# Kernel tuning notes

Hardware: AMD Instinct MI355X
Metric: run time of the kernel (lower is better)

## Reference

```python
import jax, jax.numpy as jnp
import numpy as np

B, S, H, M, STEPS = 8, 1024, 1024, 4, 5
LN_EPS = 1e-5


def _gelu(x):
    return jax.nn.gelu(x, approximate=False)  # torch nn.GELU default is exact erf


def _layernorm(x, g, b):
    mu = jnp.mean(x, axis=-1, keepdims=True)
    var = jnp.mean((x - mu) ** 2, axis=-1, keepdims=True)
    return (x - mu) * jax.lax.rsqrt(var + LN_EPS) * g + b


def setup_inputs() -> dict:
    key = jax.random.key(0)
    ks = jax.random.split(key, 16)
    def w(k, shape, scale=0.02):
        return (jax.random.normal(k, shape) * scale).astype(jnp.float32)
    z = lambda *shape: jnp.zeros(shape, jnp.float32)
    o = lambda *shape: jnp.ones(shape, jnp.float32)
    return {
        "deterministic_state": jax.random.normal(ks[0], (B, S, H), jnp.float32),
        "superposition_state": jax.random.normal(ks[1], (B, S, H * M), jnp.float32),
        "context": jax.random.normal(ks[2], (B, H), jnp.float32),
        # reasoning_mode_selector: Linear(H,H) -> GELU -> Linear(H,2) -> Softmax
        "Wm1": w(ks[3], (H, H)), "bm1": z(H), "Wm2": w(ks[4], (H, 2)), "bm2": z(2),
        # reasoning_depth_controller: Linear(H,H//2) -> GELU -> Linear(H//2,STEPS) -> Softmax
        "Wd1": w(ks[5], (H, H // 2)), "bd1": z(H // 2), "Wd2": w(ks[6], (H // 2, STEPS)), "bd2": z(STEPS),
        # explicit_reasoning_steps (stacked over STEPS): Linear(2H,H)->GELU->Linear(H,H)->LayerNorm
        "We1": w(ks[7], (STEPS, 2 * H, H)), "be1": z(STEPS, H),
        "We2": w(ks[8], (STEPS, H, H)), "be2": z(STEPS, H),
        "ln_g": o(STEPS, H), "ln_b": z(STEPS, H),
        # reasoning_memory GRUCell(H,H); gate order r,z,n as in torch
        "W_ih": w(ks[9], (H, 3 * H)), "W_hh": w(ks[10], (H, 3 * H)),
        "b_ih": z(3 * H), "b_hh": z(3 * H),
        # implicit_reasoning: Linear(H*M,2H)->GELU->Linear(2H,H*M)->LayerNorm
        "Wi1": w(ks[11], (H * M, 2 * H)), "bi1": z(2 * H),
        "Wi2": w(ks[12], (2 * H, H * M)), "bi2": z(H * M),
        "lni_g": o(H * M), "lni_b": z(H * M),
    }


def _forward(deterministic_state, superposition_state, context,
             Wm1, bm1, Wm2, bm2, Wd1, bd1, Wd2, bd2,
             We1, be1, We2, be2, ln_g, ln_b,
             W_ih, W_hh, b_ih, b_hh,
             Wi1, bi1, Wi2, bi2, lni_g, lni_b):
    b, s, h = deterministic_state.shape
    # mode / depth selection from 2D context [B,H]
    mode_weights = jax.nn.softmax(_gelu(context @ Wm1 + bm1) @ Wm2 + bm2, axis=-1)   # [B,2]
    depth_weights = jax.nn.softmax(_gelu(context @ Wd1 + bd1) @ Wd2 + bd2, axis=-1)  # [B,STEPS]

    ctx_exp = jnp.broadcast_to(context[:, None, :], (b, s, h))  # context.unsqueeze(1).expand

    def gru_cell(x, hprev):  # x,hprev: [N,H]
        gi = x @ W_ih + b_ih
        gh = hprev @ W_hh + b_hh
        i_r, i_z, i_n = jnp.split(gi, 3, axis=-1)
        h_r, h_z, h_n = jnp.split(gh, 3, axis=-1)
        r = jax.nn.sigmoid(i_r + h_r)
        z = jax.nn.sigmoid(i_z + h_z)
        n = jnp.tanh(i_n + r * h_n)
        return (1.0 - z) * n + z * hprev

    def step(carry, params):
        state, memory = carry
        W1, b1, W2, b2, g, beta = params
        combined = jnp.concatenate([state, ctx_exp], axis=-1)          # [B,S,2H]
        next_state = _layernorm(_gelu(combined @ W1 + b1) @ W2 + b2, g, beta)
        mem = gru_cell(next_state.reshape(-1, h), memory.reshape(-1, h)).reshape(b, s, h)
        gated = next_state + 0.1 * mem
        return (gated, mem), gated

    init = (deterministic_state, jnp.zeros_like(deterministic_state))
    _, gated_states = jax.lax.scan(step, init, (We1, be1, We2, be2, ln_g, ln_b))  # [STEPS,B,S,H]
    explicit_result = jnp.einsum('bi,ibsh->bsh', depth_weights, gated_states)

    implicit_result = _layernorm(_gelu(superposition_state @ Wi1 + bi1) @ Wi2 + bi2, lni_g, lni_b)  # [B,S,M*H]
    implicit_det = implicit_result.reshape(b, s, M, h).mean(axis=2)  # [B,S,H]

    result = (mode_weights[:, 0, None, None] * implicit_det
              + mode_weights[:, 1, None, None] * explicit_result)
    return result, mode_weights, depth_weights, explicit_result, implicit_result


def reference(deterministic_state, superposition_state, context,
              Wm1, bm1, Wm2, bm2, Wd1, bd1, Wd2, bd2,
              We1, be1, We2, be2, ln_g, ln_b,
              W_ih, W_hh, b_ih, b_hh,
              Wi1, bi1, Wi2, bi2, lni_g, lni_b):
    return _forward(deterministic_state, superposition_state, context,
                    Wm1, bm1, Wm2, bm2, Wd1, bd1, Wd2, bd2,
                    We1, be1, We2, be2, ln_g, ln_b,
                    W_ih, W_hh, b_ih, b_hh,
                    Wi1, bi1, Wi2, bi2, lni_g, lni_b)
```

## Files before the change

### kernel.cpp

```cpp
#include <hip/hip_runtime.h>
#include <hip/hip_bf16.h>
#include <math.h>


typedef unsigned short bf16_t;
typedef __attribute__((ext_vector_type(8))) short s8v;
typedef __attribute__((ext_vector_type(4))) float f4v;

typedef const __attribute__((address_space(1))) void* gas_ptr;
typedef __attribute__((address_space(3))) void* las_ptr;

#define DEVFN static __device__ __forceinline__

DEVFN bf16_t f2b(float f) {
    union { float f; unsigned u; } v; v.f = f;
    unsigned r = v.u + 0x7FFFu + ((v.u >> 16) & 1u);
    return (bf16_t)(r >> 16);
}
DEVFN float b2f(bf16_t b) {
    union { unsigned u; float f; } v; v.u = ((unsigned)b) << 16; return v.f;
}
DEVFN float geluf(float x) { return 0.5f * x * (1.0f + erff(x * 0.70710678118654752f)); }
DEVFN float sigmf(float x) { return 1.0f / (1.0f + expf(-x)); }

static const long OUT_RESULT = 0;
static const long OUT_MODE   = 8388608;
static const long OUT_DEPTH  = 8388624;
static const long OUT_EXPL   = 8388664;
static const long OUT_IMPL   = 16777272;

#define READ_A(h, c_) { _Pragma("unroll") \
    for (int mf = 0; mf < MF / 2; ++mf) { _Pragma("unroll") \
      for (int ks = 0; ks < 2; ++ks) { \
        aA[h][mf][ks] = *(const s8v*)(lds + (c_) * BUFB + \
            (arow_base + ((h) * (MF / 2) + mf) * 16) * 128 + \
            ((((ks << 2) + lhi) ^ l7) << 4)); } } }

#define READ_B(h, c_) { _Pragma("unroll") \
    for (int nf = 0; nf < NF / 2; ++nf) { _Pragma("unroll") \
      for (int ks = 0; ks < 2; ++ks) { \
        bB[h][nf][ks] = *(const s8v*)(lds + (c_) * BUFB + ABYTES + \
            (brow_base + ((h) * (NF / 2) + nf) * 16) * 128 + \
            ((((ks << 2) + lhi) ^ l7) << 4)); } } }

#define MFMAQ(mh, nh) { __builtin_amdgcn_s_setprio(1); _Pragma("unroll") \
    for (int mf = 0; mf < MF / 2; ++mf) { _Pragma("unroll") \
      for (int nf = 0; nf < NF / 2; ++nf) { _Pragma("unroll") \
        for (int ks = 0; ks < 2; ++ks) { \
          acc[(mh) * (MF / 2) + mf][(nh) * (NF / 2) + nf] = \
            __builtin_amdgcn_mfma_f32_16x16x32_bf16(aA[mh][mf][ks], bB[nh][nf][ks], \
                acc[(mh) * (MF / 2) + mf][(nh) * (NF / 2) + nf], 0, 0, 0); } } } \
    __builtin_amdgcn_s_setprio(0); }

#define WAIT_VM_LPT() { if (LPT == 8) asm volatile("s_waitcnt vmcnt(8)" ::: "memory"); \
                        else          asm volatile("s_waitcnt vmcnt(6)" ::: "memory"); }

template <int MF, int NF, int EPI>
__global__ __launch_bounds__(512, 2) void gemm8p(
    const bf16_t* __restrict__ A, const bf16_t* __restrict__ Bt,
    const float* __restrict__ bias, bf16_t* __restrict__ outB, int N, int K)
{
    constexpr int BM = MF * 32;
    constexpr int BN = NF * 64;
    constexpr int LA = BM / 64;
    constexpr int LB = BN / 64;
    constexpr int LPT = LA + LB;
    constexpr int ABYTES = BM * 128;
    constexpr int BUFB = (BM + BN) * 128;

    __shared__ __align__(16) char lds[2 * BUFB];

    const int tid  = threadIdx.x;
    const int lane = tid & 63;
    const int wave = tid >> 6;
    const int wm = wave >> 2, wn = wave & 3;
    const int l15 = lane & 15, lhi = lane >> 4, l7 = lane & 7;

    const int gx = gridDim.x;
    const int nwg = gx * gridDim.y;
    const int orig = blockIdx.y * gx + blockIdx.x;
    const int qq = nwg >> 3, rr8 = nwg & 7;
    const int xcd = orig & 7, lid = orig >> 3;
    const int nid = (xcd < rr8 ? xcd * (qq + 1) : rr8 * (qq + 1) + (xcd - rr8) * qq) + lid;
    const int m0 = (nid / gx) * BM;
    const int n0 = (nid % gx) * BN;

    const int NT = K >> 6;

    const int arow_base = wm * (BM / 2) + l15;
    const int brow_base = wn * (NF * 16) + l15;

    f4v acc[MF][NF];
#pragma unroll
    for (int i = 0; i < MF; ++i)
#pragma unroll
        for (int j = 0; j < NF; ++j)
#pragma unroll
            for (int q2 = 0; q2 < 4; ++q2) acc[i][j][q2] = 0.0f;

    s8v aA[2][MF / 2][2];
    s8v bB[2][NF / 2][2];

    auto stage = [&](int ts, int tb) {
        const int kt = ts << 6;
#pragma unroll
        for (int i = 0; i < LA; ++i) {
            const int li = i * 512 + tid;
            const int r = li >> 3, s = li & 7;
            const bf16_t* src = A + (long)(m0 + r) * K + kt + ((s ^ (r & 7)) << 3);
            __builtin_amdgcn_global_load_lds((gas_ptr)src, (las_ptr)(lds + tb * BUFB + li * 16), 16, 0, 0);
        }
#pragma unroll
        for (int i = 0; i < LB; ++i) {
            const int li = i * 512 + tid;
            const int r = li >> 3, s = li & 7;
            const bf16_t* src = Bt + (long)(n0 + r) * K + kt + ((s ^ (r & 7)) << 3);
            __builtin_amdgcn_global_load_lds((gas_ptr)src, (las_ptr)(lds + tb * BUFB + ABYTES + li * 16), 16, 0, 0);
        }
    };

    stage(0, 0);
    stage(1, 1);
    WAIT_VM_LPT();
    __builtin_amdgcn_sched_barrier(0);
    __builtin_amdgcn_s_barrier();
    READ_A(0, 0);
    READ_B(0, 0);

    for (int t = 0; t < NT; ++t) {
        const int c = t & 1;
        READ_A(1, c);
        READ_B(1, c);
        MFMAQ(0, 0);
        MFMAQ(1, 0);
        asm volatile("s_waitcnt lgkmcnt(0)" ::: "memory");
        __builtin_amdgcn_sched_barrier(0);
        __builtin_amdgcn_s_barrier();
        int ts = t + 2; if (ts >= NT) ts -= NT;
        stage(ts, c);
        MFMAQ(1, 1);
        WAIT_VM_LPT();
        __builtin_amdgcn_sched_barrier(0);
        __builtin_amdgcn_s_barrier();
        READ_B(0, c ^ 1);
        MFMAQ(0, 1);
        READ_A(0, c ^ 1);
    }

    const int crr = lhi << 2;
#pragma unroll
    for (int mi = 0; mi < MF; ++mi) {
#pragma unroll
        for (int ni = 0; ni < NF; ++ni) {
            const int col = n0 + wn * (NF * 16) + ni * 16 + l15;
#pragma unroll
            for (int q2 = 0; q2 < 4; ++q2) {
                const int row = m0 + wm * (BM / 2) + mi * 16 + crr + q2;
                const float v = acc[mi][ni][q2];
                if (EPI == 1) {
                    outB[(long)row * N + col] = f2b(geluf(v + bias[col]));
                } else if (EPI == 2) {
                    outB[(long)row * N + col] = f2b(geluf(v + bias[(long)(row >> 10) * N + col]));
                } else {
                    outB[(long)row * N + col] = f2b(v + bias[col]);
                }
            }
        }
    }
}

__global__ __launch_bounds__(256) void transpose_k(
    const float* __restrict__ src, bf16_t* __restrict__ dst,
    int K, int N, long sbs, long dbs)
{
    __shared__ float tile[32][33];
    const float* s = src + (long)blockIdx.z * sbs;
    bf16_t* d = dst + (long)blockIdx.z * dbs;
    const int n0 = blockIdx.x * 32, k0 = blockIdx.y * 32;
    const int tx = threadIdx.x, ty = threadIdx.y;
#pragma unroll
    for (int i = 0; i < 4; ++i)
        tile[ty + i * 8][tx] = s[(long)(k0 + ty + i * 8) * N + n0 + tx];
    __syncthreads();
#pragma unroll
    for (int i = 0; i < 4; ++i)
        d[(long)(n0 + ty + i * 8) * K + k0 + tx] = f2b(tile[tx][ty + i * 8]);
}

__global__ __launch_bounds__(256) void cvt_k(const float4* __restrict__ src,
                                             ushort4* __restrict__ dst, int n4)
{
    const int i = blockIdx.x * 256 + threadIdx.x;
    if (i < n4) {
        float4 v = src[i];
        ushort4 o; o.x = f2b(v.x); o.y = f2b(v.y); o.z = f2b(v.z); o.w = f2b(v.w);
        dst[i] = o;
    }
}

__global__ __launch_bounds__(256) void colgemv8_k(
    const float* __restrict__ ctx, const float* __restrict__ Wbase, long wts,
    int Wld, const float* __restrict__ bias, long bts,
    float* __restrict__ out, long ots, int do_gelu)
{
    __shared__ float cs[8][1024];
    __shared__ float rr[16][16][8];
    const int j0 = blockIdx.x * 16;
    const int t = blockIdx.y;
    const int tid = threadIdx.x;
    for (int i = tid; i < 2048; i += 256)
        ((float4*)cs)[i] = ((const float4*)ctx)[i];
    __syncthreads();
    const int kp = tid >> 4, jj = tid & 15;
    const float* Wp = Wbase + (long)t * wts;
    float p[8] = {0, 0, 0, 0, 0, 0, 0, 0};
    for (int i = 0; i < 64; ++i) {
        const int k = kp * 64 + i;
        const float w = Wp[(long)k * Wld + j0 + jj];
#pragma unroll
        for (int b = 0; b < 8; ++b) p[b] = fmaf(cs[b][k], w, p[b]);
    }
#pragma unroll
    for (int b = 0; b < 8; ++b) rr[kp][jj][b] = p[b];
    __syncthreads();
    if (tid < 128) {
        const int jj2 = tid >> 3, b = tid & 7;
        float s = 0.f;
#pragma unroll
        for (int k2 = 0; k2 < 16; ++k2) s += rr[k2][jj2][b];
        s += bias[(long)t * bts + j0 + jj2];
        if (do_gelu) s = geluf(s);
        out[(long)t * ots + (long)b * Wld + j0 + jj2] = s;
    }
}

__global__ __launch_bounds__(256) void selB_k(
    const float* __restrict__ h1, const float* __restrict__ hd,
    const float* __restrict__ Wm2, const float* __restrict__ bm2,
    const float* __restrict__ Wd2, const float* __restrict__ bd2,
    float* __restrict__ outM, float* __restrict__ outD,
    float* __restrict__ wsM, float* __restrict__ wsD)
{
    const int b = blockIdx.x, tid = threadIdx.x;
    __shared__ float red[256];
    float lm[2], ld[5];
    for (int o = 0; o < 2; ++o) {
        float p = 0.f;
        for (int k = tid; k < 1024; k += 256) p += h1[b * 1024 + k] * Wm2[k * 2 + o];
        red[tid] = p; __syncthreads();
        for (int s = 128; s > 0; s >>= 1) { if (tid < s) red[tid] += red[tid + s]; __syncthreads(); }
        lm[o] = red[0] + bm2[o]; __syncthreads();
    }
    for (int o = 0; o < 5; ++o) {
        float p = 0.f;
        for (int k = tid; k < 512; k += 256) p += hd[b * 512 + k] * Wd2[k * 5 + o];
        red[tid] = p; __syncthreads();
        for (int s = 128; s > 0; s >>= 1) { if (tid < s) red[tid] += red[tid + s]; __syncthreads(); }
        ld[o] = red[0] + bd2[o]; __syncthreads();
    }
    if (tid == 0) {
        float mx = fmaxf(lm[0], lm[1]);
        float e0 = expf(lm[0] - mx), e1 = expf(lm[1] - mx);
        float inv = 1.f / (e0 + e1);
        outM[b * 2] = e0 * inv; outM[b * 2 + 1] = e1 * inv;
        wsM[b * 2] = e0 * inv;  wsM[b * 2 + 1] = e1 * inv;
        float md = ld[0];
        for (int o = 1; o < 5; ++o) md = fmaxf(md, ld[o]);
        float es[5]; float sum = 0.f;
        for (int o = 0; o < 5; ++o) { es[o] = expf(ld[o] - md); sum += es[o]; }
        for (int o = 0; o < 5; ++o) { outD[b * 5 + o] = es[o] / sum; wsD[b * 5 + o] = es[o] / sum; }
    }
}

__global__ __launch_bounds__(256) void ln1024_k(
    const bf16_t* __restrict__ X, const float* __restrict__ g,
    const float* __restrict__ b, bf16_t* __restrict__ Yb)
{
    const int row = blockIdx.x, tid = threadIdx.x;
    const ushort4 xv = ((const ushort4*)(X + (long)row * 1024))[tid];
    const float x0 = b2f(xv.x), x1 = b2f(xv.y), x2 = b2f(xv.z), x3 = b2f(xv.w);
    float s = x0 + x1 + x2 + x3;
    float ss = x0 * x0 + x1 * x1 + x2 * x2 + x3 * x3;
#pragma unroll
    for (int o = 32; o > 0; o >>= 1) { s += __shfl_down(s, o); ss += __shfl_down(ss, o); }
    __shared__ float rs[4], rss[4];
    const int wv = tid >> 6, ln = tid & 63;
    if (ln == 0) { rs[wv] = s; rss[wv] = ss; }
    __syncthreads();
    const float S = rs[0] + rs[1] + rs[2] + rs[3];
    const float SS = rss[0] + rss[1] + rss[2] + rss[3];
    const float mean = S * (1.0f / 1024.0f);
    const float var = SS * (1.0f / 1024.0f) - mean * mean;
    const float rstd = rsqrtf(var + 1e-5f);
    const float4 gv = ((const float4*)g)[tid];
    const float4 bv = ((const float4*)b)[tid];
    ushort4 ob;
    ob.x = f2b((x0 - mean) * rstd * gv.x + bv.x);
    ob.y = f2b((x1 - mean) * rstd * gv.y + bv.y);
    ob.z = f2b((x2 - mean) * rstd * gv.z + bv.z);
    ob.w = f2b((x3 - mean) * rstd * gv.w + bv.w);
    ((ushort4*)(Yb + (long)row * 1024))[tid] = ob;
}

template <bool FIRST>
__global__ __launch_bounds__(256) void gru_k(
    const bf16_t* __restrict__ gi, const bf16_t* __restrict__ gh,
    const float* __restrict__ bhh, const bf16_t* __restrict__ nsB,
    bf16_t* __restrict__ memB, bf16_t* __restrict__ stateB,
    float* __restrict__ expl, const float* __restrict__ depthw, int t)
{
    const long i4 = (long)blockIdx.x * 256 + threadIdx.x;
    const long row = i4 >> 8;
    const int h4 = (int)(i4 & 255) << 2;
    const bf16_t* gir = gi + row * 3072 + h4;
    const ushort4 vir = *(const ushort4*)(gir);
    const ushort4 viz = *(const ushort4*)(gir + 1024);
    const ushort4 vin = *(const ushort4*)(gir + 2048);
    float hr[4], hz[4], hn[4];
    if (FIRST) {
        const float4 a = *(const float4*)(bhh + h4);
        const float4 c = *(const float4*)(bhh + 1024 + h4);
        const float4 d = *(const float4*)(bhh + 2048 + h4);
        hr[0] = a.x; hr[1] = a.y; hr[2] = a.z; hr[3] = a.w;
        hz[0] = c.x; hz[1] = c.y; hz[2] = c.z; hz[3] = c.w;
        hn[0] = d.x; hn[1] = d.y; hn[2] = d.z; hn[3] = d.w;
    } else {
        const bf16_t* ghr = gh + row * 3072 + h4;
        const ushort4 g1 = *(const ushort4*)(ghr);
        const ushort4 g2 = *(const ushort4*)(ghr + 1024);
        const ushort4 g3 = *(const ushort4*)(ghr + 2048);
        hr[0] = b2f(g1.x); hr[1] = b2f(g1.y); hr[2] = b2f(g1.z); hr[3] = b2f(g1.w);
        hz[0] = b2f(g2.x); hz[1] = b2f(g2.y); hz[2] = b2f(g2.z); hz[3] = b2f(g2.w);
        hn[0] = b2f(g3.x); hn[1] = b2f(g3.y); hn[2] = b2f(g3.z); hn[3] = b2f(g3.w);
    }
    const ushort4 nsv = *(const ushort4*)(nsB + row * 1024 + h4);
    float mo[4] = {0.f, 0.f, 0.f, 0.f};
    if (!FIRST) {
        const ushort4 mv = *(const ushort4*)(memB + row * 1024 + h4);
        mo[0] = b2f(mv.x); mo[1] = b2f(mv.y); mo[2] = b2f(mv.z); mo[3] = b2f(mv.w);
    }
    const float dw = depthw[(int)(row >> 10) * 5 + t];
    const float ir[4] = {b2f(vir.x), b2f(vir.y), b2f(vir.z), b2f(vir.w)};
    const float iz[4] = {b2f(viz.x), b2f(viz.y), b2f(viz.z), b2f(viz.w)};
    const float in_[4] = {b2f(vin.x), b2f(vin.y), b2f(vin.z), b2f(vin.w)};
    const float ns[4] = {b2f(nsv.x), b2f(nsv.y), b2f(nsv.z), b2f(nsv.w)};
    ushort4 mnb, stb; float4 exv;
    float mn[4], gt[4];
#pragma unroll
    for (int i = 0; i < 4; ++i) {
        const float rg = sigmf(ir[i] + hr[i]);
        const float zg = sigmf(iz[i] + hz[i]);
        const float ng = tanhf(in_[i] + rg * hn[i]);
        mn[i] = (1.0f - zg) * ng + zg * mo[i];
        gt[i] = ns[i] + 0.1f * mn[i];
    }
    mnb.x = f2b(mn[0]); mnb.y = f2b(mn[1]); mnb.z = f2b(mn[2]); mnb.w = f2b(mn[3]);
    stb.x = f2b(gt[0]); stb.y = f2b(gt[1]); stb.z = f2b(gt[2]); stb.w = f2b(gt[3]);
    exv.x = dw * gt[0]; exv.y = dw * gt[1]; exv.z = dw * gt[2]; exv.w = dw * gt[3];
    *(ushort4*)(memB + row * 1024 + h4) = mnb;
    *(ushort4*)(stateB + row * 1024 + h4) = stb;
    float* ep = expl + row * 1024 + h4;
    if (FIRST) {
        *(float4*)ep = exv;
    } else {
        float4 old = *(const float4*)ep;
        old.x += exv.x; old.y += exv.y; old.z += exv.z; old.w += exv.w;
        *(float4*)ep = old;
    }
}

__global__ __launch_bounds__(1024) void ln4096_final_k(
    const bf16_t* __restrict__ Ypre, const float* __restrict__ g,
    const float* __restrict__ b, const float* __restrict__ expl,
    float* __restrict__ implOut, float* __restrict__ result,
    const float* __restrict__ modew)
{
    const int row = blockIdx.x, tid = threadIdx.x;
    const ushort4 xv = ((const ushort4*)(Ypre + (long)row * 4096))[tid];
    const float x0 = b2f(xv.x), x1 = b2f(xv.y), x2 = b2f(xv.z), x3 = b2f(xv.w);
    float s = x0 + x1 + x2 + x3;
    float ss = x0 * x0 + x1 * x1 + x2 * x2 + x3 * x3;
#pragma unroll
    for (int o = 32; o > 0; o >>= 1) { s += __shfl_down(s, o); ss += __shfl_down(ss, o); }
    __shared__ float rs[16], rss[16];
    __shared__ float ylds[4096];
    const int wv = tid >> 6, ln = tid & 63;
    if (ln == 0) { rs[wv] = s; rss[wv] = ss; }
    __syncthreads();
    if (tid < 64) {
        float a = (ln < 16) ? rs[ln] : 0.f;
        float c2 = (ln < 16) ? rss[ln] : 0.f;
#pragma unroll
        for (int o = 8; o > 0; o >>= 1) { a += __shfl_down(a, o); c2 += __shfl_down(c2, o); }
        if (ln == 0) { rs[0] = a; rss[0] = c2; }
    }
    __syncthreads();
    const float mean = rs[0] * (1.f / 4096.f);
    const float var = rss[0] * (1.f / 4096.f) - mean * mean;
    const float rstd = rsqrtf(var + 1e-5f);
    const float4 gv = ((const float4*)g)[tid];
    const float4 bv = ((const float4*)b)[tid];
    float4 y;
    y.x = (x0 - mean) * rstd * gv.x + bv.x;
    y.y = (x1 - mean) * rstd * gv.y + bv.y;
    y.z = (x2 - mean) * rstd * gv.z + bv.z;
    y.w = (x3 - mean) * rstd * gv.w + bv.w;
    ((float4*)(implOut + (long)row * 4096))[tid] = y;
    ((float4*)ylds)[tid] = y;
    __syncthreads();
    const int bidx = row >> 10;
    const float det4 = 0.25f * (ylds[tid] + ylds[tid + 1024] + ylds[tid + 2048] + ylds[tid + 3072]);
    result[(long)row * 1024 + tid] = modew[bidx * 2] * det4
                                   + modew[bidx * 2 + 1] * expl[(long)row * 1024 + tid];
}

extern "C" void kernel_launch(void* const* d_in, const int* in_sizes, int n_in,
                              void* d_out, int out_size, void* d_ws, size_t ws_size,
                              hipStream_t stream)
{
    const float* det    = (const float*)d_in[0];
    const float* super_ = (const float*)d_in[1];
    const float* ctx    = (const float*)d_in[2];
    const float* Wm1 = (const float*)d_in[3];
    const float* bm1 = (const float*)d_in[4];
    const float* Wm2 = (const float*)d_in[5];
    const float* bm2 = (const float*)d_in[6];
    const float* Wd1 = (const float*)d_in[7];
    const float* bd1 = (const float*)d_in[8];
    const float* Wd2 = (const float*)d_in[9];
    const float* bd2 = (const float*)d_in[10];
    const float* We1 = (const float*)d_in[11];
    const float* be1 = (const float*)d_in[12];
    const float* We2 = (const float*)d_in[13];
    const float* be2 = (const float*)d_in[14];
    const float* ln_g = (const float*)d_in[15];
    const float* ln_b = (const float*)d_in[16];
    const float* W_ih = (const float*)d_in[17];
    const float* W_hh = (const float*)d_in[18];
    const float* b_ih = (const float*)d_in[19];
    const float* b_hh = (const float*)d_in[20];
    const float* Wi1 = (const float*)d_in[21];
    const float* bi1 = (const float*)d_in[22];
    const float* Wi2 = (const float*)d_in[23];
    const float* bi2 = (const float*)d_in[24];
    const float* lni_g = (const float*)d_in[25];
    const float* lni_b = (const float*)d_in[26];

    float* out = (float*)d_out;
    char* W = (char*)d_ws;

    bf16_t* We1sT = (bf16_t*)(W + 0);
    bf16_t* We2T  = (bf16_t*)(W + 10485760L);
    bf16_t* WihT  = (bf16_t*)(W + 20971520L);
    bf16_t* WhhT  = (bf16_t*)(W + 27262976L);
    bf16_t* Wi1T  = (bf16_t*)(W + 33554432L);
    bf16_t* Wi2T  = (bf16_t*)(W + 50331648L);
    float* ctxbias = (float*)(W + 67108864L);
    float* modew   = (float*)(W + 67272704L);
    float* depthw  = (float*)(W + 67272768L);
    float* h1ws    = (float*)(W + 67276800L);
    float* hdws    = (float*)(W + 67309568L);
    const long SB = 67325952L;
    bf16_t* stateb = (bf16_t*)(W + SB);
    bf16_t* Zb     = (bf16_t*)(W + SB + 16777216L);
    bf16_t* memb   = (bf16_t*)(W + SB + 50331648L);
    bf16_t* nsB    = (bf16_t*)(W + SB + 67108864L);
    bf16_t* gi     = (bf16_t*)(W + SB + 83886080L);
    bf16_t* gh     = (bf16_t*)(W + SB + 134217728L);
    bf16_t* Y1     = gi;
    bf16_t* superb = gi;
    bf16_t* Yi     = (bf16_t*)(W + SB + 83886080L + 67108864L);
    bf16_t* Ypre   = gi;

    (void)in_sizes; (void)n_in; (void)out_size; (void)ws_size;

    dim3 tb(32, 8);

    colgemv8_k<<<dim3(64, 1), 256, 0, stream>>>(ctx, Wm1, 0, 1024, bm1, 0, h1ws, 0, 1);
    colgemv8_k<<<dim3(32, 1), 256, 0, stream>>>(ctx, Wd1, 0, 512, bd1, 0, hdws, 0, 1);
    colgemv8_k<<<dim3(64, 5), 256, 0, stream>>>(ctx, We1 + 1048576L, 2097152L, 1024,
                                                be1, 1024, ctxbias, 8192, 0);
    selB_k<<<8, 256, 0, stream>>>(h1ws, hdws, Wm2, bm2, Wd2, bd2,
                                  out + OUT_MODE, out + OUT_DEPTH, modew, depthw);

    transpose_k<<<dim3(32, 32, 5), tb, 0, stream>>>(We1, We1sT, 1024, 1024, 2097152L, 1048576L);
    transpose_k<<<dim3(32, 32, 5), tb, 0, stream>>>(We2, We2T, 1024, 1024, 1048576L, 1048576L);
    transpose_k<<<dim3(96, 32, 1), tb, 0, stream>>>(W_ih, WihT, 1024, 3072, 0L, 0L);
    transpose_k<<<dim3(96, 32, 1), tb, 0, stream>>>(W_hh, WhhT, 1024, 3072, 0L, 0L);
    transpose_k<<<dim3(64, 128, 1), tb, 0, stream>>>(Wi1, Wi1T, 4096, 2048, 0L, 0L);
    transpose_k<<<dim3(128, 64, 1), tb, 0, stream>>>(Wi2, Wi2T, 2048, 4096, 0L, 0L);

    cvt_k<<<8192, 256, 0, stream>>>((const float4*)det, (ushort4*)stateb, 2097152);

    for (int t = 0; t < 5; ++t) {
        gemm8p<4, 4, 2><<<dim3(4, 64), 512, 0, stream>>>(stateb, We1sT + (long)t * 1048576,
                                                         ctxbias + (long)t * 8192, Y1, 1024, 1024);
        gemm8p<4, 4, 3><<<dim3(4, 64), 512, 0, stream>>>(Y1, We2T + (long)t * 1048576,
                                                         be2 + t * 1024, Zb, 1024, 1024);
        ln1024_k<<<8192, 256, 0, stream>>>(Zb, ln_g + t * 1024, ln_b + t * 1024, nsB);
        gemm8p<4, 4, 3><<<dim3(12, 64), 512, 0, stream>>>(nsB, WihT, b_ih, gi, 3072, 1024);
        if (t > 0)
            gemm8p<4, 4, 3><<<dim3(12, 64), 512, 0, stream>>>(memb, WhhT, b_hh, gh, 3072, 1024);
        if (t == 0)
            gru_k<true><<<8192, 256, 0, stream>>>(gi, gh, b_hh, nsB, memb, stateb,
                                                  out + OUT_EXPL, depthw, t);
        else
            gru_k<false><<<8192, 256, 0, stream>>>(gi, gh, b_hh, nsB, memb, stateb,
                                                   out + OUT_EXPL, depthw, t);
    }

    cvt_k<<<32768, 256, 0, stream>>>((const float4*)super_, (ushort4*)superb, 8388608);
    gemm8p<8, 4, 1><<<dim3(8, 32), 512, 0, stream>>>(superb, Wi1T, bi1, Yi, 2048, 4096);
    gemm8p<8, 4, 3><<<dim3(16, 32), 512, 0, stream>>>(Yi, Wi2T, bi2, Ypre, 4096, 2048);
    ln4096_final_k<<<8192, 1024, 0, stream>>>(Ypre, lni_g, lni_b, out + OUT_EXPL,
                                              out + OUT_IMPL, out + OUT_RESULT, modew);
}
```

Before: 1.459 ms.

## Restructure GEMM main loop into four-phase quadrant schedule with split staging

Rewrites the bf16 MFMA GEMM inner loop into four phases. Each phase computes one quadrant of the wave's output tile, keeping a single A register set and two B register sets. Global-to-LDS staging of the next tile is split into A and B halves and spread across the phases, with finer vmcnt waits and extra barriers. The wave-to-tile mapping also changes so each wave covers interleaved halves of the block. The aim is better overlap of LDS reads, global loads and MFMA work with less register pressure, at the cost of more barriers per iteration.

```diff
diff --git a/kernel.cpp b/kernel.cpp
--- a/kernel.cpp
+++ b/kernel.cpp
@@ -22,6 +22,18 @@
 }
 DEVFN float geluf(float x) { return 0.5f * x * (1.0f + erff(x * 0.70710678118654752f)); }
 DEVFN float sigmf(float x) { return 1.0f / (1.0f + expf(-x)); }
+
+template <int N_> DEVFN void waitvm() {
+    if constexpr (N_ == 7)  asm volatile("s_waitcnt vmcnt(7)"  ::: "memory");
+    if constexpr (N_ == 9)  asm volatile("s_waitcnt vmcnt(9)"  ::: "memory");
+    if constexpr (N_ == 10) asm volatile("s_waitcnt vmcnt(10)" ::: "memory");
+    if constexpr (N_ == 12) asm volatile("s_waitcnt vmcnt(12)" ::: "memory");
+    __builtin_amdgcn_sched_barrier(0);
+}
+DEVFN void lgkm0() {
+    asm volatile("s_waitcnt lgkmcnt(0)" ::: "memory");
+    __builtin_amdgcn_sched_barrier(0);
+}
 
 static const long OUT_RESULT = 0;
 static const long OUT_MODE   = 8388608;
@@ -29,31 +41,28 @@
 static const long OUT_EXPL   = 8388664;
 static const long OUT_IMPL   = 16777272;
 
-#define READ_A(h, c_) { _Pragma("unroll") \
+#define READ_AH(mh, c_) { _Pragma("unroll") \
     for (int mf = 0; mf < MF / 2; ++mf) { _Pragma("unroll") \
       for (int ks = 0; ks < 2; ++ks) { \
-        aA[h][mf][ks] = *(const s8v*)(lds + (c_) * BUFB + \
-            (arow_base + ((h) * (MF / 2) + mf) * 16) * 128 + \
+        aR[mf][ks] = *(const s8v*)(lds + (c_) * BUFB + \
+            ((mh) * (BM / 2) + wm * (BM / 4) + mf * 16 + l15) * 128 + \
             ((((ks << 2) + lhi) ^ l7) << 4)); } } }
 
-#define READ_B(h, c_) { _Pragma("unroll") \
+#define READ_BH(nh, c_, dst) { _Pragma("unroll") \
     for (int nf = 0; nf < NF / 2; ++nf) { _Pragma("unroll") \
       for (int ks = 0; ks < 2; ++ks) { \
-        bB[h][nf][ks] = *(const s8v*)(lds + (c_) * BUFB + ABYTES + \
-            (brow_base + ((h) * (NF / 2) + nf) * 16) * 128 + \
+        dst[nf][ks] = *(const s8v*)(lds + (c_) * BUFB + ABYTES + \
+            ((nh) * (BN / 2) + wn * (BN / 8) + nf * 16 + l15) * 128 + \
             ((((ks << 2) + lhi) ^ l7) << 4)); } } }
 
-#define MFMAQ(mh, nh) { __builtin_amdgcn_s_setprio(1); _Pragma("unroll") \
+#define MFMA_Q(mh, nh, bset) { __builtin_amdgcn_s_setprio(1); _Pragma("unroll") \
     for (int mf = 0; mf < MF / 2; ++mf) { _Pragma("unroll") \
       for (int nf = 0; nf < NF / 2; ++nf) { _Pragma("unroll") \
         for (int ks = 0; ks < 2; ++ks) { \
           acc[(mh) * (MF / 2) + mf][(nh) * (NF / 2) + nf] = \
-            __builtin_amdgcn_mfma_f32_16x16x32_bf16(aA[mh][mf][ks], bB[nh][nf][ks], \
+            __builtin_amdgcn_mfma_f32_16x16x32_bf16(aR[mf][ks], bset[nf][ks], \
                 acc[(mh) * (MF / 2) + mf][(nh) * (NF / 2) + nf], 0, 0, 0); } } } \
     __builtin_amdgcn_s_setprio(0); }
-
-#define WAIT_VM_LPT() { if (LPT == 8) asm volatile("s_waitcnt vmcnt(8)" ::: "memory"); \
-                        else          asm volatile("s_waitcnt vmcnt(6)" ::: "memory"); }
 
 template <int MF, int NF, int EPI>
 __global__ __launch_bounds__(512, 2) void gemm8p(
@@ -64,7 +73,10 @@
     constexpr int BN = NF * 64;
     constexpr int LA = BM / 64;
     constexpr int LB = BN / 64;
-    constexpr int LPT = LA + LB;
+    constexpr int sA = LA / 2;
+    constexpr int sB = LB / 2;
+    constexpr int V1 = 3 * sA + 2 * sB;
+    constexpr int V24 = 3 * (sA + sB);
     constexpr int ABYTES = BM * 128;
     constexpr int BUFB = (BM + BN) * 128;
 
@@ -87,9 +99,6 @@
 
     const int NT = K >> 6;
 
-    const int arow_base = wm * (BM / 2) + l15;
-    const int brow_base = wn * (NF * 16) + l15;
-
     f4v acc[MF][NF];
 #pragma unroll
     for (int i = 0; i < MF; ++i)
@@ -98,71 +107,87 @@
 #pragma unroll
             for (int q2 = 0; q2 < 4; ++q2) acc[i][j][q2] = 0.0f;
 
-    s8v aA[2][MF / 2][2];
-    s8v bB[2][NF / 2][2];
-
-    auto stage = [&](int ts, int tb) {
+    s8v aR[MF / 2][2];
+    s8v bR0[NF / 2][2], bR1[NF / 2][2];
+
+    auto stageA = [&](int ts, int tb, int h) {
         const int kt = ts << 6;
 #pragma unroll
-        for (int i = 0; i < LA; ++i) {
-            const int li = i * 512 + tid;
+        for (int i = 0; i < sA; ++i) {
+            const int li = (h * sA + i) * 512 + tid;
             const int r = li >> 3, s = li & 7;
             const bf16_t* src = A + (long)(m0 + r) * K + kt + ((s ^ (r & 7)) << 3);
             __builtin_amdgcn_global_load_lds((gas_ptr)src, (las_ptr)(lds + tb * BUFB + li * 16), 16, 0, 0);
         }
-#pragma unroll
-        for (int i = 0; i < LB; ++i) {
-            const int li = i * 512 + tid;
+    };
+    auto stageB = [&](int ts, int tb, int h) {
+        const int kt = ts << 6;
+#pragma unroll
+        for (int i = 0; i < sB; ++i) {
+            const int li = (h * sB + i) * 512 + tid;
             const int r = li >> 3, s = li & 7;
             const bf16_t* src = Bt + (long)(n0 + r) * K + kt + ((s ^ (r & 7)) << 3);
             __builtin_amdgcn_global_load_lds((gas_ptr)src, (las_ptr)(lds + tb * BUFB + ABYTES + li * 16), 16, 0, 0);
         }
     };
 
-    stage(0, 0);
-    stage(1, 1);
-    WAIT_VM_LPT();
-    __builtin_amdgcn_sched_barrier(0);
+    stageA(0, 0, 0); stageB(0, 0, 0); stageB(0, 0, 1); stageA(0, 0, 1);
+    stageA(1, 1, 0); stageB(1, 1, 0); stageB(1, 1, 1); stageA(1, 1, 1);
+    waitvm<V24>();
     __builtin_amdgcn_s_barrier();
-    READ_A(0, 0);
-    READ_B(0, 0);
 
     for (int t = 0; t < NT; ++t) {
         const int c = t & 1;
-        READ_A(1, c);
-        READ_B(1, c);
-        MFMAQ(0, 0);
-        MFMAQ(1, 0);
-        asm volatile("s_waitcnt lgkmcnt(0)" ::: "memory");
-        __builtin_amdgcn_sched_barrier(0);
-        __builtin_amdgcn_s_barrier();
         int ts = t + 2; if (ts >= NT) ts -= NT;
-        stage(ts, c);
-        MFMAQ(1, 1);
-        WAIT_VM_LPT();
-        __builtin_amdgcn_sched_barrier(0);
-        __builtin_amdgcn_s_barrier();
-        READ_B(0, c ^ 1);
-        MFMAQ(0, 1);
-        READ_A(0, c ^ 1);
+        READ_AH(0, c);
+        READ_BH(0, c, bR0);
+        waitvm<V1>();
+        __builtin_amdgcn_s_barrier();
+        lgkm0();
+        MFMA_Q(0, 0, bR0);
+        __builtin_amdgcn_s_barrier();
+        READ_BH(1, c, bR1);
+        stageA(ts, c, 0); stageB(ts, c, 0);
+        waitvm<V24>();
+        __builtin_amdgcn_s_barrier();
+        lgkm0();
+        MFMA_Q(0, 1, bR1);
+        __builtin_amdgcn_s_barrier();
+        READ_AH(1, c);
+        stageB(ts, c, 1);
+        __builtin_amdgcn_s_barrier();
+        lgkm0();
+        MFMA_Q(1, 1, bR1);
+        __builtin_amdgcn_s_barrier();
+        stageA(ts, c, 1);
+        waitvm<V24>();
+        __builtin_amdgcn_s_barrier();
+        MFMA_Q(1, 0, bR0);
+        __builtin_amdgcn_s_barrier();
     }
 
     const int crr = lhi << 2;
 #pragma unroll
-    for (int mi = 0; mi < MF; ++mi) {
-#pragma unroll
-        for (int ni = 0; ni < NF; ++ni) {
-            const int col = n0 + wn * (NF * 16) + ni * 16 + l15;
-#pragma unroll
-            for (int q2 = 0; q2 < 4; ++q2) {
-                const int row = m0 + wm * (BM / 2) + mi * 16 + crr + q2;
-                const float v = acc[mi][ni][q2];
-                if (EPI == 1) {
-                    outB[(long)row * N + col] = f2b(geluf(v + bias[col]));
-                } else if (EPI == 2) {
-                    outB[(long)row * N + col] = f2b(geluf(v + bias[(long)(row >> 10) * N + col]));
-                } else {
-                    outB[(long)row * N + col] = f2b(v + bias[col]);
+    for (int mh = 0; mh < 2; ++mh) {
+#pragma unroll
+        for (int mf = 0; mf < MF / 2; ++mf) {
+#pragma unroll
+            for (int nh = 0; nh < 2; ++nh) {
+#pragma unroll
+                for (int nf = 0; nf < NF / 2; ++nf) {
+                    const int col = n0 + nh * (BN / 2) + wn * (BN / 8) + nf * 16 + l15;
+#pragma unroll
+                    for (int q2 = 0; q2 < 4; ++q2) {
+                        const int row = m0 + mh * (BM / 2) + wm * (BM / 4) + mf * 16 + crr + q2;
+                        const float v = acc[mh * (MF / 2) + mf][nh * (NF / 2) + nf][q2];
+                        if (EPI == 1) {
+                            outB[(long)row * N + col] = f2b(geluf(v + bias[col]));
+                        } else if (EPI == 2) {
+                            outB[(long)row * N + col] = f2b(geluf(v + bias[(long)(row >> 10) * N + col]));
+                        } else {
+                            outB[(long)row * N + col] = f2b(v + bias[col]);
+                        }
+                    }
                 }
             }
         }
```

Result: no change. 1.482 ms (+1.6%).

## Batch GRU input/hidden GEMMs in one launch and defer explicit accumulation

Applied to the files above, without the earlier changes.

The W_ih and W_hh GRU gate GEMMs now run as a single launch, with blockIdx.z selecting which operand set each block uses. This doubles the grid and removes one launch per step. The GRU kernel no longer does a read-modify-write of the fp32 explicit accumulator each step. Instead, each step's gated state is kept in its own bf16 slab, and the final layernorm kernel sums the five slabs with the depth weights. This cuts fp32 traffic per step but needs a larger workspace and more reads in the final kernel.

```diff
diff --git a/kernel.cpp b/kernel.cpp
--- a/kernel.cpp
+++ b/kernel.cpp
@@ -28,6 +28,8 @@
 static const long OUT_DEPTH  = 8388624;
 static const long OUT_EXPL   = 8388664;
 static const long OUT_IMPL   = 16777272;
+
+static const long SLAB = 8388608;
 
 #define READ_A(h, c_) { _Pragma("unroll") \
     for (int mf = 0; mf < MF / 2; ++mf) { _Pragma("unroll") \
@@ -57,8 +59,11 @@
 
 template <int MF, int NF, int EPI>
 __global__ __launch_bounds__(512, 2) void gemm8p(
-    const bf16_t* __restrict__ A, const bf16_t* __restrict__ Bt,
-    const float* __restrict__ bias, bf16_t* __restrict__ outB, int N, int K)
+    const bf16_t* __restrict__ A0, const bf16_t* __restrict__ Bt0,
+    const float* __restrict__ bias0, bf16_t* __restrict__ out0,
+    const bf16_t* __restrict__ A1, const bf16_t* __restrict__ Bt1,
+    const float* __restrict__ bias1, bf16_t* __restrict__ out1,
+    int N, int K)
 {
     constexpr int BM = MF * 32;
     constexpr int BN = NF * 64;
@@ -69,6 +74,11 @@
     constexpr int BUFB = (BM + BN) * 128;
 
     __shared__ __align__(16) char lds[2 * BUFB];
+
+    const bf16_t* A    = blockIdx.z ? A1 : A0;
+    const bf16_t* Bt   = blockIdx.z ? Bt1 : Bt0;
+    const float*  bias = blockIdx.z ? bias1 : bias0;
+    bf16_t*       outB = blockIdx.z ? out1 : out0;
 
     const int tid  = threadIdx.x;
     const int lane = tid & 63;
@@ -152,7 +162,7 @@
     for (int mi = 0; mi < MF; ++mi) {
 #pragma unroll
         for (int ni = 0; ni < NF; ++ni) {
-            const int col = n0 + wn * (NF * 16) + ni * 16 + l15;
+            const int col = n0 + wn * (NF * 16) + ni * 16 + (lane & 15);
 #pragma unroll
             for (int q2 = 0; q2 < 4; ++q2) {
                 const int row = m0 + wm * (BM / 2) + mi * 16 + crr + q2;
@@ -306,8 +316,7 @@
 __global__ __launch_bounds__(256) void gru_k(
     const bf16_t* __restrict__ gi, const bf16_t* __restrict__ gh,
     const float* __restrict__ bhh, const bf16_t* __restrict__ nsB,
-    bf16_t* __restrict__ memB, bf16_t* __restrict__ stateB,
-    float* __restrict__ expl, const float* __restrict__ depthw, int t)
+    bf16_t* __restrict__ memB, bf16_t* __restrict__ stateOut)
 {
     const long i4 = (long)blockIdx.x * 256 + threadIdx.x;
     const long row = i4 >> 8;
@@ -339,12 +348,11 @@
         const ushort4 mv = *(const ushort4*)(memB + row * 1024 + h4);
         mo[0] = b2f(mv.x); mo[1] = b2f(mv.y); mo[2] = b2f(mv.z); mo[3] = b2f(mv.w);
     }
-    const float dw = depthw[(int)(row >> 10) * 5 + t];
     const float ir[4] = {b2f(vir.x), b2f(vir.y), b2f(vir.z), b2f(vir.w)};
     const float iz[4] = {b2f(viz.x), b2f(viz.y), b2f(viz.z), b2f(viz.w)};
     const float in_[4] = {b2f(vin.x), b2f(vin.y), b2f(vin.z), b2f(vin.w)};
     const float ns[4] = {b2f(nsv.x), b2f(nsv.y), b2f(nsv.z), b2f(nsv.w)};
-    ushort4 mnb, stb; float4 exv;
+    ushort4 mnb, stb;
     float mn[4], gt[4];
 #pragma unroll
     for (int i = 0; i < 4; ++i) {
@@ -356,23 +364,15 @@
     }
     mnb.x = f2b(mn[0]); mnb.y = f2b(mn[1]); mnb.z = f2b(mn[2]); mnb.w = f2b(mn[3]);
     stb.x = f2b(gt[0]); stb.y = f2b(gt[1]); stb.z = f2b(gt[2]); stb.w = f2b(gt[3]);
-    exv.x = dw * gt[0]; exv.y = dw * gt[1]; exv.z = dw * gt[2]; exv.w = dw * gt[3];
     *(ushort4*)(memB + row * 1024 + h4) = mnb;
-    *(ushort4*)(stateB + row * 1024 + h4) = stb;
-    float* ep = expl + row * 1024 + h4;
-    if (FIRST) {
-        *(float4*)ep = exv;
-    } else {
-        float4 old = *(const float4*)ep;
-        old.x += exv.x; old.y += exv.y; old.z += exv.z; old.w += exv.w;
-        *(float4*)ep = old;
-    }
+    *(ushort4*)(stateOut + row * 1024 + h4) = stb;
 }
 
 __global__ __launch_bounds__(1024) void ln4096_final_k(
     const bf16_t* __restrict__ Ypre, const float* __restrict__ g,
-    const float* __restrict__ b, const float* __restrict__ expl,
-    float* __restrict__ implOut, float* __restrict__ result,
+    const float* __restrict__ b, const bf16_t* __restrict__ stS,
+    const float* __restrict__ depthw, float* __restrict__ implOut,
+    float* __restrict__ explOut, float* __restrict__ result,
     const float* __restrict__ modew)
 {
     const int row = blockIdx.x, tid = threadIdx.x;
@@ -409,9 +409,14 @@
     ((float4*)ylds)[tid] = y;
     __syncthreads();
     const int bidx = row >> 10;
+    const long off = (long)row * 1024 + tid;
+    float ex = 0.f;
+#pragma unroll
+    for (int tt = 0; tt < 5; ++tt)
+        ex += depthw[bidx * 5 + tt] * b2f(stS[(long)tt * SLAB + off]);
+    explOut[off] = ex;
     const float det4 = 0.25f * (ylds[tid] + ylds[tid + 1024] + ylds[tid + 2048] + ylds[tid + 3072]);
-    result[(long)row * 1024 + tid] = modew[bidx * 2] * det4
-                                   + modew[bidx * 2 + 1] * expl[(long)row * 1024 + tid];
+    result[off] = modew[bidx * 2] * det4 + modew[bidx * 2 + 1] * ex;
 }
 
 extern "C" void kernel_launch(void* const* d_in, const int* in_sizes, int n_in,
@@ -461,15 +466,15 @@
     float* h1ws    = (float*)(W + 67276800L);
     float* hdws    = (float*)(W + 67309568L);
     const long SB = 67325952L;
-    bf16_t* stateb = (bf16_t*)(W + SB);
-    bf16_t* Zb     = (bf16_t*)(W + SB + 16777216L);
-    bf16_t* memb   = (bf16_t*)(W + SB + 50331648L);
-    bf16_t* nsB    = (bf16_t*)(W + SB + 67108864L);
-    bf16_t* gi     = (bf16_t*)(W + SB + 83886080L);
-    bf16_t* gh     = (bf16_t*)(W + SB + 134217728L);
+    bf16_t* stateS = (bf16_t*)(W + SB);
+    bf16_t* Zb     = (bf16_t*)(W + SB + 100663296L);
+    bf16_t* memb   = (bf16_t*)(W + SB + 117440512L);
+    bf16_t* nsB    = (bf16_t*)(W + SB + 134217728L);
+    bf16_t* gi     = (bf16_t*)(W + SB + 150994944L);
+    bf16_t* gh     = (bf16_t*)(W + SB + 201326592L);
     bf16_t* Y1     = gi;
     bf16_t* superb = gi;
-    bf16_t* Yi     = (bf16_t*)(W + SB + 83886080L + 67108864L);
+    bf16_t* Yi     = (bf16_t*)(W + SB + 201326592L + 16777216L);
     bf16_t* Ypre   = gi;
 
     (void)in_sizes; (void)n_in; (void)out_size; (void)ws_size;
@@ -490,28 +495,38 @@
     transpose_k<<<dim3(64, 128, 1), tb, 0, stream>>>(Wi1, Wi1T, 4096, 2048, 0L, 0L);
     transpose_k<<<dim3(128, 64, 1), tb, 0, stream>>>(Wi2, Wi2T, 2048, 4096, 0L, 0L);
 
-    cvt_k<<<8192, 256, 0, stream>>>((const float4*)det, (ushort4*)stateb, 2097152);
+    cvt_k<<<8192, 256, 0, stream>>>((const float4*)det, (ushort4*)stateS, 2097152);
 
     for (int t = 0; t < 5; ++t) {
-        gemm8p<4, 4, 2><<<dim3(4, 64), 512, 0, stream>>>(stateb, We1sT + (long)t * 1048576,
-                                                         ctxbias + (long)t * 8192, Y1, 1024, 1024);
-        gemm8p<4, 4, 3><<<dim3(4, 64), 512, 0, stream>>>(Y1, We2T + (long)t * 1048576,
-                                                         be2 + t * 1024, Zb, 1024, 1024);
+        const bf16_t* stIn = stateS + (long)t * SLAB;
+        bf16_t* stOut = stateS + (long)(t + 1) * SLAB;
+        gemm8p<4, 4, 2><<<dim3(4, 64, 1), 512, 0, stream>>>(
+            stIn, We1sT + (long)t * 1048576, ctxbias + (long)t * 8192, Y1,
+            stIn, We1sT + (long)t * 1048576, ctxbias + (long)t * 8192, Y1, 1024, 1024);
+        gemm8p<4, 4, 3><<<dim3(4, 64, 1), 512, 0, stream>>>(
+            Y1, We2T + (long)t * 1048576, be2 + t * 1024, Zb,
+            Y1, We2T + (long)t * 1048576, be2 + t * 1024, Zb, 1024, 1024);
         ln1024_k<<<8192, 256, 0, stream>>>(Zb, ln_g + t * 1024, ln_b + t * 1024, nsB);
-        gemm8p<4, 4, 3><<<dim3(12, 64), 512, 0, stream>>>(nsB, WihT, b_ih, gi, 3072, 1024);
         if (t > 0)
-            gemm8p<4, 4, 3><<<dim3(12, 64), 512, 0, stream>>>(memb, WhhT, b_hh, gh, 3072, 1024);
+            gemm8p<4, 4, 3><<<dim3(12, 64, 2), 512, 0, stream>>>(
+                nsB, WihT, b_ih, gi,
+                memb, WhhT, b_hh, gh, 3072, 1024);
+        else
+            gemm8p<4, 4, 3><<<dim3(12, 64, 1), 512, 0, stream>>>(
+                nsB, WihT, b_ih, gi,
+                nsB, WihT, b_ih, gi, 3072, 1024);
         if (t == 0)
-            gru_k<true><<<8192, 256, 0, stream>>>(gi, gh, b_hh, nsB, memb, stateb,
-                                                  out + OUT_EXPL, depthw, t);
+            gru_k<true><<<8192, 256, 0, stream>>>(gi, gh, b_hh, nsB, memb, stOut);
         else
-            gru_k<false><<<8192, 256, 0, stream>>>(gi, gh, b_hh, nsB, memb, stateb,
-                                                   out + OUT_EXPL, depthw, t);
+            gru_k<false><<<8192, 256, 0, stream>>>(gi, gh, b_hh, nsB, memb, stOut);
     }
 
     cvt_k<<<32768, 256, 0, stream>>>((const float4*)super_, (ushort4*)superb, 8388608);
-    gemm8p<8, 4, 1><<<dim3(8, 32), 512, 0, stream>>>(superb, Wi1T, bi1, Yi, 2048, 4096);
-    gemm8p<8, 4, 3><<<dim3(16, 32), 512, 0, stream>>>(Yi, Wi2T, bi2, Ypre, 4096, 2048);
-    ln4096_final_k<<<8192, 1024, 0, stream>>>(Ypre, lni_g, lni_b, out + OUT_EXPL,
-                                              out + OUT_IMPL, out + OUT_RESULT, modew);
-}
+    gemm8p<8, 4, 1><<<dim3(8, 32, 1), 512, 0, stream>>>(
+        superb, Wi1T, bi1, Yi, superb, Wi1T, bi1, Yi, 2048, 4096);
+    gemm8p<8, 4, 3><<<dim3(16, 32, 1), 512, 0, stream>>>(
+        Yi, Wi2T, bi2, Ypre, Yi, Wi2T, bi2, Ypre, 4096, 2048);
+    ln4096_final_k<<<8192, 1024, 0, stream>>>(Ypre, lni_g, lni_b, stateS + SLAB, depthw,
+                                              out + OUT_IMPL, out + OUT_EXPL,
+                                              out + OUT_RESULT, modew);
+}
```

Result: faster. 1.429 ms, median of 2 (-2.0%).
